# Optimization experiments

Measured on AMD Instinct MI355X. Metric: run time of the kernel, lower is better.

Reference implementation:

```python
import jax, jax.numpy as jnp
import numpy as np

B, S, D = 4, 2048, 1024


def setup_inputs() -> dict:
    key = jax.random.key(0)
    ks = jax.random.split(key, 7)
    s = 1.0 / np.sqrt(D)
    return {
        "x": jax.random.normal(ks[0], (B, S, D), dtype=jnp.float32),
        "Wq": jax.random.normal(ks[1], (D, D), dtype=jnp.float32) * s,
        "bq": jnp.zeros((D,), dtype=jnp.float32),
        "Wk": jax.random.normal(ks[2], (D, D), dtype=jnp.float32) * s,
        "bk": jnp.zeros((D,), dtype=jnp.float32),
        "Wv": jax.random.normal(ks[3], (D, D), dtype=jnp.float32) * s,
        "bv": jnp.zeros((D,), dtype=jnp.float32),
    }


def reference(x, Wq, bq, Wk, bk, Wv, bv):
    # Linear layers: x @ W^T + b (torch nn.Linear convention)
    Q = jnp.einsum("bsd,ed->bse", x, Wq) + bq
    K = jnp.einsum("bsd,ed->bse", x, Wk) + bk
    V = jnp.einsum("bsd,ed->bse", x, Wv) + bv
    scale = 1.0 / (x.shape[-1] ** 0.5)
    scores = jnp.einsum("bse,bte->bst", Q, K) * scale  # [B, S, S]
    attn = jax.nn.softmax(scores, axis=-1)
    out = jnp.einsum("bst,bte->bse", attn, V)
    return out
```

## Files before the change

kernel.cpp:

```cpp
#include <hip/hip_runtime.h>
#include <math.h>


typedef _Float16 f16;
typedef _Float16 f16x8 __attribute__((ext_vector_type(8)));
typedef _Float16 f16x4 __attribute__((ext_vector_type(4)));
typedef float f32x4 __attribute__((ext_vector_type(4)));

__device__ __forceinline__ void glds16(const void* g, const void* l) {
    __builtin_amdgcn_global_load_lds(
        (const __attribute__((address_space(1))) void*)g,
        (__attribute__((address_space(3))) void*)l, 16, 0, 0);
}

__global__ __launch_bounds__(256) void cvt16_kernel(
    const float* __restrict__ in, f16* __restrict__ o, int n4)
{
    int i = blockIdx.x * 256 + threadIdx.x;
    if (i >= n4) return;
    float4 v = ((const float4*)in)[i];
    f16x4 h = { (f16)v.x, (f16)v.y, (f16)v.z, (f16)v.w };
    ((f16x4*)o)[i] = h;
}

__global__ __launch_bounds__(256) void cvtw_kernel(
    const float* __restrict__ Wq, const float* __restrict__ Wk,
    const float* __restrict__ Wv, f16* __restrict__ o, int n4)
{
    int i = blockIdx.x * 256 + threadIdx.x;
    if (i >= n4) return;
    const float* src = (blockIdx.y == 0) ? Wq : (blockIdx.y == 1) ? Wk : Wv;
    float4 v = ((const float4*)src)[i];
    f16x4 h = { (f16)v.x, (f16)v.y, (f16)v.z, (f16)v.w };
    ((f16x4*)(o + (size_t)blockIdx.y * 1024 * 1024))[i] = h;
}

__global__ __launch_bounds__(256) void zero_kernel(float* __restrict__ p, int n)
{
    int i = blockIdx.x * 256 + threadIdx.x;
    if (i < n) p[i] = 0.0f;
}

#define ABUF 16384
#define BBUF 8192
#define BOFF 49152

__device__ __forceinline__ void mfma_core3(
    const f16* __restrict__ A, int lda,
    const f16* __restrict__ B, int ldb,
    int K, int m0, int n0, f16* sm, f32x4 acc[4][4])
{
    const int tid  = threadIdx.x;
    const int lane = tid & 63;
    const int w    = tid >> 6;
    const int wr   = w >> 1;
    const int wc   = w & 1;
    const int lr   = lane & 15;
    const int kq   = lane >> 4;

    const int rl = lane >> 3;
    const int ch = (lane & 7) ^ rl;

    const f16* gA[4];
    #pragma unroll
    for (int p = 0; p < 4; ++p)
        gA[p] = A + (size_t)(m0 + p * 64 + w * 8 + rl) * lda + ch * 8;
    const f16* gB[2];
    #pragma unroll
    for (int p = 0; p < 2; ++p)
        gB[p] = B + (size_t)(n0 + p * 64 + w * 8 + rl) * ldb + ch * 8;

    const int NT = K >> 6;

    #pragma unroll
    for (int s = 0; s < 2; ++s) {
        f16* lA = sm + s * ABUF + w * 8 * 64;
        f16* lB = sm + BOFF + s * BBUF + w * 8 * 64;
        #pragma unroll
        for (int p = 0; p < 4; ++p) glds16(gA[p] + s * 64, lA + p * 4096);
        #pragma unroll
        for (int p = 0; p < 2; ++p) glds16(gB[p] + s * 64, lB + p * 4096);
    }

    int kst = 128, sb = 2, cur = 0;
    for (int t = 0; t < NT; ++t) {
        if (t + 2 < NT) {
            f16* lA = sm + sb * ABUF + w * 8 * 64;
            f16* lB = sm + BOFF + sb * BBUF + w * 8 * 64;
            #pragma unroll
            for (int p = 0; p < 4; ++p) glds16(gA[p] + kst, lA + p * 4096);
            #pragma unroll
            for (int p = 0; p < 2; ++p) glds16(gB[p] + kst, lB + p * 4096);
            kst += 64;
            sb = (sb == 2) ? 0 : sb + 1;
        }
        if (t + 2 < NT)      asm volatile("s_waitcnt vmcnt(12)" ::: "memory");
        else if (t + 1 < NT) asm volatile("s_waitcnt vmcnt(6)"  ::: "memory");
        else                 asm volatile("s_waitcnt vmcnt(0)"  ::: "memory");
        asm volatile("s_barrier" ::: "memory");

        const f16* sA = sm + cur * ABUF;
        const f16* sB = sm + BOFF + cur * BBUF;
        #pragma unroll
        for (int kk = 0; kk < 2; ++kk) {
            f16x8 a[4], b[4];
            const int c = kk * 4 + kq;
            #pragma unroll
            for (int i = 0; i < 4; ++i) {
                const int ar = wr * 64 + i * 16 + lr;
                a[i] = *(const f16x8*)&sA[ar * 64 + ((c ^ (ar & 7)) * 8)];
            }
            #pragma unroll
            for (int j = 0; j < 4; ++j) {
                const int br = wc * 64 + j * 16 + lr;
                b[j] = *(const f16x8*)&sB[br * 64 + ((c ^ (br & 7)) * 8)];
            }
            asm volatile("s_waitcnt lgkmcnt(0)" ::: "memory");
            __builtin_amdgcn_sched_barrier(0);
            __builtin_amdgcn_s_setprio(1);
            #pragma unroll
            for (int i = 0; i < 4; ++i)
                #pragma unroll
                for (int j = 0; j < 4; ++j)
                    acc[i][j] = __builtin_amdgcn_mfma_f32_16x16x32_f16(a[i], b[j], acc[i][j], 0, 0, 0);
            __builtin_amdgcn_s_setprio(0);
            asm volatile("s_barrier" ::: "memory");
        }
        cur = (cur == 2) ? 0 : cur + 1;
    }
}

__global__ __launch_bounds__(512) void qkv_mfma_kernel(
    const f16* __restrict__ xh, const f16* __restrict__ Wh,
    const float* __restrict__ bq, const float* __restrict__ bk,
    const float* __restrict__ bv,
    f16* __restrict__ Qh, f16* __restrict__ Kh, f16* __restrict__ Vh)
{
    extern __shared__ __align__(16) f16 smem[];
    int flat = blockIdx.x + 8 * (blockIdx.y + 32 * blockIdx.z);
    flat = (flat & 7) * 96 + (flat >> 3);
    const int bx = flat & 7;
    const int by = (flat >> 3) & 31;
    const int bz = flat >> 8;

    const int m0 = by * 256;
    const int n0 = bx * 128;

    f32x4 acc[4][4];
    #pragma unroll
    for (int i = 0; i < 4; ++i)
        #pragma unroll
        for (int j = 0; j < 4; ++j) acc[i][j] = (f32x4){0.f, 0.f, 0.f, 0.f};

    mfma_core3(xh, 1024, Wh + (size_t)bz * 1024 * 1024, 1024, 1024, m0, n0, smem, acc);

    const float* bias = (bz == 0) ? bq : (bz == 1) ? bk : bv;
    const float  sc   = (bz == 0) ? 0.03125f : 1.0f;
    f16* C = (bz == 0) ? Qh : (bz == 1) ? Kh : Vh;
    const int lane = threadIdx.x & 63;
    const int w    = threadIdx.x >> 6;
    const int wr = w >> 1, wc = w & 1;
    const int col  = lane & 15;
    const int quad = lane >> 4;

    #pragma unroll
    for (int j = 0; j < 4; ++j) {
        const int gn = n0 + wc * 64 + j * 16 + col;
        const float bb = bias[gn];
        #pragma unroll
        for (int i = 0; i < 4; ++i)
            #pragma unroll
            for (int r = 0; r < 4; ++r) {
                const int gm = m0 + wr * 64 + i * 16 + quad * 4 + r;
                C[(size_t)gm * 1024 + gn] = (f16)((acc[i][j][r] + bb) * sc);
            }
    }
}

__global__ __launch_bounds__(256) void vtrans_kernel(
    const f16* __restrict__ V, f16* __restrict__ Vt)
{
    __shared__ f16 t[64][72];
    const int b  = blockIdx.z;
    const int s0 = blockIdx.x * 64;
    const int d0 = blockIdx.y * 64;
    const int tid = threadIdx.x;

    const int r  = tid >> 3;
    const int c8 = (tid & 7) * 8;
    const f16* src = V + ((size_t)b * 2048 + s0) * 1024 + d0;
    *(f16x8*)&t[r][c8]      = *(const f16x8*)(src + (size_t)r * 1024 + c8);
    *(f16x8*)&t[r + 32][c8] = *(const f16x8*)(src + (size_t)(r + 32) * 1024 + c8);
    __syncthreads();

    const int dl  = tid >> 2;
    const int sl0 = (tid & 3) * 16;
    f16* dst = Vt + ((size_t)b * 1024 + d0 + dl) * 2048 + s0 + sl0;
    f16 buf[16];
    #pragma unroll
    for (int u = 0; u < 16; ++u) buf[u] = t[sl0 + u][dl];
    *(f16x8*)dst       = *(f16x8*)&buf[0];
    *(f16x8*)(dst + 8) = *(f16x8*)&buf[8];
}

__global__ __launch_bounds__(512) void scores_exp_kernel(
    const f16* __restrict__ Qh, const f16* __restrict__ Kh,
    f16* __restrict__ P, float* __restrict__ sums)
{
    extern __shared__ __align__(16) f16 smem[];
    const int b  = blockIdx.z;
    const int m0 = blockIdx.y * 256;
    const int n0 = blockIdx.x * 128;

    f32x4 acc[4][4];
    #pragma unroll
    for (int i = 0; i < 4; ++i)
        #pragma unroll
        for (int j = 0; j < 4; ++j) acc[i][j] = (f32x4){0.f, 0.f, 0.f, 0.f};

    const size_t ao = (size_t)b * 2048 * 1024;
    mfma_core3(Qh + ao, 1024, Kh + ao, 1024, 1024, m0, n0, smem, acc);

    const int lane = threadIdx.x & 63;
    const int w    = threadIdx.x >> 6;
    const int wr = w >> 1, wc = w & 1;
    const int col  = lane & 15;
    const int quad = lane >> 4;
    f16* C = P + (size_t)b * 2048 * 2048;

    float rp[4][4];
    #pragma unroll
    for (int i = 0; i < 4; ++i)
        #pragma unroll
        for (int r = 0; r < 4; ++r) rp[i][r] = 0.0f;

    #pragma unroll
    for (int i = 0; i < 4; ++i)
        #pragma unroll
        for (int r = 0; r < 4; ++r) {
            const int gm = m0 + wr * 64 + i * 16 + quad * 4 + r;
            #pragma unroll
            for (int j = 0; j < 4; ++j) {
                const int gn = n0 + wc * 64 + j * 16 + col;
                const f16 p = (f16)__expf(acc[i][j][r]);
                C[(size_t)gm * 2048 + gn] = p;
                rp[i][r] += (float)p;
            }
        }

    #pragma unroll
    for (int i = 0; i < 4; ++i)
        #pragma unroll
        for (int r = 0; r < 4; ++r) {
            float v = rp[i][r];
            v += __shfl_xor(v, 1);
            v += __shfl_xor(v, 2);
            v += __shfl_xor(v, 4);
            v += __shfl_xor(v, 8);
            rp[i][r] = v;
        }
    if (col == 0) {
        #pragma unroll
        for (int i = 0; i < 4; ++i)
            #pragma unroll
            for (int r = 0; r < 4; ++r) {
                const int row = m0 + wr * 64 + i * 16 + quad * 4 + r;
                atomicAdd(&sums[b * 2048 + row], rp[i][r]);
            }
    }
}

__global__ __launch_bounds__(512) void pv_mfma_kernel(
    const f16* __restrict__ P, const f16* __restrict__ Vt,
    const float* __restrict__ sums, float* __restrict__ out)
{
    extern __shared__ __align__(16) f16 smem[];
    const int b  = blockIdx.z;
    const int m0 = blockIdx.y * 256;
    const int n0 = blockIdx.x * 128;

    f32x4 acc[4][4];
    #pragma unroll
    for (int i = 0; i < 4; ++i)
        #pragma unroll
        for (int j = 0; j < 4; ++j) acc[i][j] = (f32x4){0.f, 0.f, 0.f, 0.f};

    const size_t ao = (size_t)b * 2048 * 2048;
    const size_t bo = (size_t)b * 1024 * 2048;
    mfma_core3(P + ao, 2048, Vt + bo, 2048, 2048, m0, n0, smem, acc);

    const int lane = threadIdx.x & 63;
    const int w    = threadIdx.x >> 6;
    const int wr = w >> 1, wc = w & 1;
    const int col  = lane & 15;
    const int quad = lane >> 4;
    float* C = out + (size_t)b * 2048 * 1024;

    #pragma unroll
    for (int i = 0; i < 4; ++i)
        #pragma unroll
        for (int r = 0; r < 4; ++r) {
            const int rowg = m0 + wr * 64 + i * 16 + quad * 4 + r;
            const float inv = 1.0f / sums[b * 2048 + rowg];
            #pragma unroll
            for (int j = 0; j < 4; ++j) {
                const int gn = n0 + wc * 64 + j * 16 + col;
                C[(size_t)rowg * 1024 + gn] = acc[i][j][r] * inv;
            }
        }
}

extern "C" void kernel_launch(void* const* d_in, const int* in_sizes, int n_in,
                              void* d_out, int out_size, void* d_ws, size_t ws_size,
                              hipStream_t stream)
{
    (void)in_sizes; (void)n_in; (void)out_size; (void)ws_size;
    const int Bn = 4, S = 2048, D = 1024;
    const float* x  = (const float*)d_in[0];
    const float* Wq = (const float*)d_in[1];
    const float* bq = (const float*)d_in[2];
    const float* Wk = (const float*)d_in[3];
    const float* bk = (const float*)d_in[4];
    const float* Wv = (const float*)d_in[5];
    const float* bv = (const float*)d_in[6];
    float* out = (float*)d_out;

    const size_t MB = 1024 * 1024;
    char* w = (char*)d_ws;
    f16*   xh   = (f16*)(w + 0 * MB);
    f16*   Wh3  = (f16*)(w + 16 * MB);
    f16*   Vh   = (f16*)(w + 22 * MB);
    f16*   Qh   = (f16*)(w + 38 * MB);
    f16*   Kh   = (f16*)(w + 54 * MB);
    f16*   Vt   = (f16*)(w + 70 * MB);
    float* sums = (float*)(w + 86 * MB);
    f16*   P    = (f16*)(w + 0 * MB);

    static bool attr_set = false;
    if (!attr_set) {
        hipFuncSetAttribute(reinterpret_cast<const void*>(qkv_mfma_kernel),
                            hipFuncAttributeMaxDynamicSharedMemorySize, 147456);
        hipFuncSetAttribute(reinterpret_cast<const void*>(scores_exp_kernel),
                            hipFuncAttributeMaxDynamicSharedMemorySize, 147456);
        hipFuncSetAttribute(reinterpret_cast<const void*>(pv_mfma_kernel),
                            hipFuncAttributeMaxDynamicSharedMemorySize, 147456);
        attr_set = true;
    }

    cvt16_kernel<<<dim3(Bn * S * D / 4 / 256), 256, 0, stream>>>(x, xh, Bn * S * D / 4);
    cvtw_kernel<<<dim3(D * D / 4 / 256, 3), 256, 0, stream>>>(Wq, Wk, Wv, Wh3, D * D / 4);
    zero_kernel<<<dim3((Bn * S + 255) / 256), 256, 0, stream>>>(sums, Bn * S);

    qkv_mfma_kernel<<<dim3(D / 128, (Bn * S) / 256, 3), 512, 147456, stream>>>(
        xh, Wh3, bq, bk, bv, Qh, Kh, Vh);
    vtrans_kernel<<<dim3(S / 64, D / 64, Bn), 256, 0, stream>>>(Vh, Vt);

    scores_exp_kernel<<<dim3(S / 128, S / 256, Bn), 512, 147456, stream>>>(
        Qh, Kh, P, sums);
    pv_mfma_kernel<<<dim3(D / 128, S / 256, Bn), 512, 147456, stream>>>(
        P, Vt, sums, out);
}
```

Measured before the change: 267.1 us.

## Software-pipeline LDS fragment reads with MFMA and swizzle block order for L2 locality

Restructures the shared GEMM mainloop so the next tile's LDS fragments are read into registers while MFMAs run on the current tile, using double register buffers and a two-step unrolled loop with rotating LDS stage pointers. It also remaps block indices in the scores and PV kernels into an XCD-aware interleaved order, and adds a min-waves-per-EU hint of 2 to launch bounds. The aim is to hide LDS latency and raise cache locality, at the cost of more registers, which could conflict with the occupancy hint and cause spills. Shared memory of 144 KB per block may already limit residency to one block per CU.

```diff
diff --git a/kernel.cpp b/kernel.cpp
--- a/kernel.cpp
+++ b/kernel.cpp
@@ -12,6 +12,11 @@
         (const __attribute__((address_space(1))) void*)g,
         (__attribute__((address_space(3))) void*)l, 16, 0, 0);
 }
+
+#define VMCNT(n)  asm volatile("s_waitcnt vmcnt(" #n ")" ::: "memory")
+#define LGKM(n)   asm volatile("s_waitcnt lgkmcnt(" #n ")" ::: "memory")
+#define BARRIER() asm volatile("s_barrier" ::: "memory")
+#define SCHEDB()  __builtin_amdgcn_sched_barrier(0)
 
 __global__ __launch_bounds__(256) void cvt16_kernel(
     const float* __restrict__ in, f16* __restrict__ o, int n4)
@@ -44,6 +49,38 @@
 #define ABUF 16384
 #define BBUF 8192
 #define BOFF 49152
+
+__device__ __forceinline__ void frag_read16(
+    const f16* __restrict__ sA, const f16* __restrict__ sB,
+    int wr, int wc, int lr, int kq, f16x8 a[2][4], f16x8 b[2][4])
+{
+    #pragma unroll
+    for (int kk = 0; kk < 2; ++kk) {
+        const int c = kk * 4 + kq;
+        #pragma unroll
+        for (int i = 0; i < 4; ++i) {
+            const int ar = wr * 64 + i * 16 + lr;
+            a[kk][i] = *(const f16x8*)&sA[ar * 64 + ((c ^ (ar & 7)) * 8)];
+        }
+        #pragma unroll
+        for (int j = 0; j < 4; ++j) {
+            const int br = wc * 64 + j * 16 + lr;
+            b[kk][j] = *(const f16x8*)&sB[br * 64 + ((c ^ (br & 7)) * 8)];
+        }
+    }
+}
+
+__device__ __forceinline__ void mfma32(
+    const f16x8 a[2][4], const f16x8 b[2][4], f32x4 acc[4][4])
+{
+    #pragma unroll
+    for (int kk = 0; kk < 2; ++kk)
+        #pragma unroll
+        for (int i = 0; i < 4; ++i)
+            #pragma unroll
+            for (int j = 0; j < 4; ++j)
+                acc[i][j] = __builtin_amdgcn_mfma_f32_16x16x32_f16(a[kk][i], b[kk][j], acc[i][j], 0, 0, 0);
+}
 
 __device__ __forceinline__ void mfma_core3(
     const f16* __restrict__ A, int lda,
@@ -72,65 +109,62 @@
 
     const int NT = K >> 6;
 
-    #pragma unroll
-    for (int s = 0; s < 2; ++s) {
-        f16* lA = sm + s * ABUF + w * 8 * 64;
-        f16* lB = sm + BOFF + s * BBUF + w * 8 * 64;
-        #pragma unroll
-        for (int p = 0; p < 4; ++p) glds16(gA[p] + s * 64, lA + p * 4096);
-        #pragma unroll
-        for (int p = 0; p < 2; ++p) glds16(gB[p] + s * 64, lB + p * 4096);
+    f16* sA0 = sm;             f16* sB0 = sm + BOFF;
+    f16* sA1 = sm + ABUF;      f16* sB1 = sm + BOFF + BBUF;
+    f16* sA2 = sm + 2 * ABUF;  f16* sB2 = sm + BOFF + 2 * BBUF;
+
+    #define STAGE(kofs, dA, dB) do {                                          \
+        _Pragma("unroll")                                                     \
+        for (int p = 0; p < 4; ++p)                                           \
+            glds16(gA[p] + (kofs), (dA) + w * 512 + p * 4096);                \
+        _Pragma("unroll")                                                     \
+        for (int p = 0; p < 2; ++p)                                           \
+            glds16(gB[p] + (kofs), (dB) + w * 512 + p * 4096);                \
+    } while (0)
+
+    STAGE(0,  sA0, sB0);
+    STAGE(64, sA1, sB1);
+    VMCNT(6);
+    BARRIER();
+    f16x8 a0[2][4], b0[2][4], a1[2][4], b1[2][4];
+    frag_read16(sA0, sB0, wr, wc, lr, kq, a0, b0);
+
+    for (int t = 0; t < NT; t += 2) {
+        if (t + 2 < NT) { STAGE((t + 2) * 64, sA2, sB2); VMCNT(6); }
+        else            { VMCNT(0); }
+        BARRIER();
+        frag_read16(sA1, sB1, wr, wc, lr, kq, a1, b1);
+        LGKM(15);
+        SCHEDB();
+        __builtin_amdgcn_s_setprio(1);
+        mfma32(a0, b0, acc);
+        __builtin_amdgcn_s_setprio(0);
+        BARRIER();
+
+        if (t + 3 < NT) { STAGE((t + 3) * 64, sA0, sB0); }
+        if (t + 2 < NT) {
+            if (t + 3 < NT) { VMCNT(6); } else { VMCNT(0); }
+        }
+        BARRIER();
+        if (t + 2 < NT) {
+            frag_read16(sA2, sB2, wr, wc, lr, kq, a0, b0);
+            LGKM(15);
+        } else {
+            LGKM(0);
+        }
+        SCHEDB();
+        __builtin_amdgcn_s_setprio(1);
+        mfma32(a1, b1, acc);
+        __builtin_amdgcn_s_setprio(0);
+        BARRIER();
+
+        f16* tA = sA2; sA2 = sA1; sA1 = sA0; sA0 = tA;
+        f16* tB = sB2; sB2 = sB1; sB1 = sB0; sB0 = tB;
     }
-
-    int kst = 128, sb = 2, cur = 0;
-    for (int t = 0; t < NT; ++t) {
-        if (t + 2 < NT) {
-            f16* lA = sm + sb * ABUF + w * 8 * 64;
-            f16* lB = sm + BOFF + sb * BBUF + w * 8 * 64;
-            #pragma unroll
-            for (int p = 0; p < 4; ++p) glds16(gA[p] + kst, lA + p * 4096);
-            #pragma unroll
-            for (int p = 0; p < 2; ++p) glds16(gB[p] + kst, lB + p * 4096);
-            kst += 64;
-            sb = (sb == 2) ? 0 : sb + 1;
-        }
-        if (t + 2 < NT)      asm volatile("s_waitcnt vmcnt(12)" ::: "memory");
-        else if (t + 1 < NT) asm volatile("s_waitcnt vmcnt(6)"  ::: "memory");
-        else                 asm volatile("s_waitcnt vmcnt(0)"  ::: "memory");
-        asm volatile("s_barrier" ::: "memory");
-
-        const f16* sA = sm + cur * ABUF;
-        const f16* sB = sm + BOFF + cur * BBUF;
-        #pragma unroll
-        for (int kk = 0; kk < 2; ++kk) {
-            f16x8 a[4], b[4];
-            const int c = kk * 4 + kq;
-            #pragma unroll
-            for (int i = 0; i < 4; ++i) {
-                const int ar = wr * 64 + i * 16 + lr;
-                a[i] = *(const f16x8*)&sA[ar * 64 + ((c ^ (ar & 7)) * 8)];
-            }
-            #pragma unroll
-            for (int j = 0; j < 4; ++j) {
-                const int br = wc * 64 + j * 16 + lr;
-                b[j] = *(const f16x8*)&sB[br * 64 + ((c ^ (br & 7)) * 8)];
-            }
-            asm volatile("s_waitcnt lgkmcnt(0)" ::: "memory");
-            __builtin_amdgcn_sched_barrier(0);
-            __builtin_amdgcn_s_setprio(1);
-            #pragma unroll
-            for (int i = 0; i < 4; ++i)
-                #pragma unroll
-                for (int j = 0; j < 4; ++j)
-                    acc[i][j] = __builtin_amdgcn_mfma_f32_16x16x32_f16(a[i], b[j], acc[i][j], 0, 0, 0);
-            __builtin_amdgcn_s_setprio(0);
-            asm volatile("s_barrier" ::: "memory");
-        }
-        cur = (cur == 2) ? 0 : cur + 1;
-    }
-}
-
-__global__ __launch_bounds__(512) void qkv_mfma_kernel(
+    #undef STAGE
+}
+
+__global__ __launch_bounds__(512, 2) void qkv_mfma_kernel(
     const f16* __restrict__ xh, const f16* __restrict__ Wh,
     const float* __restrict__ bq, const float* __restrict__ bk,
     const float* __restrict__ bv,
@@ -203,14 +237,19 @@
     *(f16x8*)(dst + 8) = *(f16x8*)&buf[8];
 }
 
-__global__ __launch_bounds__(512) void scores_exp_kernel(
+__global__ __launch_bounds__(512, 2) void scores_exp_kernel(
     const f16* __restrict__ Qh, const f16* __restrict__ Kh,
     f16* __restrict__ P, float* __restrict__ sums)
 {
     extern __shared__ __align__(16) f16 smem[];
-    const int b  = blockIdx.z;
-    const int m0 = blockIdx.y * 256;
-    const int n0 = blockIdx.x * 128;
+    int flat = blockIdx.x + 16 * (blockIdx.y + 8 * blockIdx.z);
+    flat = (flat & 7) * 64 + (flat >> 3);
+    const int bx = flat & 15;
+    const int by = (flat >> 4) & 7;
+    const int b  = flat >> 7;
+
+    const int m0 = by * 256;
+    const int n0 = bx * 128;
 
     f32x4 acc[4][4];
     #pragma unroll
@@ -270,14 +309,19 @@
     }
 }
 
-__global__ __launch_bounds__(512) void pv_mfma_kernel(
+__global__ __launch_bounds__(512, 2) void pv_mfma_kernel(
     const f16* __restrict__ P, const f16* __restrict__ Vt,
     const float* __restrict__ sums, float* __restrict__ out)
 {
     extern __shared__ __align__(16) f16 smem[];
-    const int b  = blockIdx.z;
-    const int m0 = blockIdx.y * 256;
-    const int n0 = blockIdx.x * 128;
+    int flat = blockIdx.x + 8 * (blockIdx.y + 8 * blockIdx.z);
+    flat = (flat & 7) * 32 + (flat >> 3);
+    const int bx = flat & 7;
+    const int by = (flat >> 3) & 7;
+    const int b  = flat >> 6;
+
+    const int m0 = by * 256;
+    const int n0 = bx * 128;
 
     f32x4 acc[4][4];
     #pragma unroll
@@ -338,11 +382,11 @@
 
     static bool attr_set = false;
     if (!attr_set) {
-        hipFuncSetAttribute(reinterpret_cast<const void*>(qkv_mfma_kernel),
+        (void)hipFuncSetAttribute(reinterpret_cast<const void*>(qkv_mfma_kernel),
                             hipFuncAttributeMaxDynamicSharedMemorySize, 147456);
-        hipFuncSetAttribute(reinterpret_cast<const void*>(scores_exp_kernel),
+        (void)hipFuncSetAttribute(reinterpret_cast<const void*>(scores_exp_kernel),
                             hipFuncAttributeMaxDynamicSharedMemorySize, 147456);
-        hipFuncSetAttribute(reinterpret_cast<const void*>(pv_mfma_kernel),
+        (void)hipFuncSetAttribute(reinterpret_cast<const void*>(pv_mfma_kernel),
                             hipFuncAttributeMaxDynamicSharedMemorySize, 147456);
         attr_set = true;
     }
```

New measurement: 267.9 us. About the same (+0.3%).

## Fuse prep kernels and write V transposed directly from QKV epilogue

Applied to the files above, without the earlier changes.

Merges the x/W fp16 conversion and the sums zeroing into one prep kernel, cutting two launches. The QKV GEMM epilogue for the V plane now writes V transposed (f16x4 along sequence) straight into Vt, removing the separate transpose kernel and the round trip of V through memory. The mfma pipeline swaps buffer-index arithmetic for rotating pointers. The transposed stores are strided by 2048 elements per column, which may coalesce worse than the old row-major writes.

```diff
diff --git a/kernel.cpp b/kernel.cpp
--- a/kernel.cpp
+++ b/kernel.cpp
@@ -13,32 +13,36 @@
         (__attribute__((address_space(3))) void*)l, 16, 0, 0);
 }
 
-__global__ __launch_bounds__(256) void cvt16_kernel(
-    const float* __restrict__ in, f16* __restrict__ o, int n4)
-{
-    int i = blockIdx.x * 256 + threadIdx.x;
-    if (i >= n4) return;
-    float4 v = ((const float4*)in)[i];
-    f16x4 h = { (f16)v.x, (f16)v.y, (f16)v.z, (f16)v.w };
-    ((f16x4*)o)[i] = h;
-}
-
-__global__ __launch_bounds__(256) void cvtw_kernel(
+#define VMCNT(n)  asm volatile("s_waitcnt vmcnt(" #n ")" ::: "memory")
+#define LGKM(n)   asm volatile("s_waitcnt lgkmcnt(" #n ")" ::: "memory")
+#define BARRIER() asm volatile("s_barrier" ::: "memory")
+#define SCHEDB()  __builtin_amdgcn_sched_barrier(0)
+
+__global__ __launch_bounds__(256) void prep_kernel(
+    const float* __restrict__ x,
     const float* __restrict__ Wq, const float* __restrict__ Wk,
-    const float* __restrict__ Wv, f16* __restrict__ o, int n4)
-{
-    int i = blockIdx.x * 256 + threadIdx.x;
-    if (i >= n4) return;
-    const float* src = (blockIdx.y == 0) ? Wq : (blockIdx.y == 1) ? Wk : Wv;
-    float4 v = ((const float4*)src)[i];
-    f16x4 h = { (f16)v.x, (f16)v.y, (f16)v.z, (f16)v.w };
-    ((f16x4*)(o + (size_t)blockIdx.y * 1024 * 1024))[i] = h;
-}
-
-__global__ __launch_bounds__(256) void zero_kernel(float* __restrict__ p, int n)
-{
-    int i = blockIdx.x * 256 + threadIdx.x;
-    if (i < n) p[i] = 0.0f;
+    const float* __restrict__ Wv,
+    f16* __restrict__ xh, f16* __restrict__ Wh3, float* __restrict__ sums)
+{
+    const int bid = blockIdx.x, tid = threadIdx.x;
+    if (bid < 8) {
+        float4 z = {0.f, 0.f, 0.f, 0.f};
+        ((float4*)sums)[bid * 256 + tid] = z;
+    }
+    if (bid < 8192) {
+        const int i = bid * 256 + tid;
+        float4 v = ((const float4*)x)[i];
+        f16x4 h = { (f16)v.x, (f16)v.y, (f16)v.z, (f16)v.w };
+        ((f16x4*)xh)[i] = h;
+    } else {
+        const int wid   = bid - 8192;
+        const int plane = wid >> 10;
+        const int i     = (wid & 1023) * 256 + tid;
+        const float* src = (plane == 0) ? Wq : (plane == 1) ? Wk : Wv;
+        float4 v = ((const float4*)src)[i];
+        f16x4 h = { (f16)v.x, (f16)v.y, (f16)v.z, (f16)v.w };
+        ((f16x4*)(Wh3 + (size_t)plane * 1024 * 1024))[i] = h;
+    }
 }
 
 #define ABUF 16384
@@ -72,51 +76,55 @@
 
     const int NT = K >> 6;
 
-    #pragma unroll
-    for (int s = 0; s < 2; ++s) {
-        f16* lA = sm + s * ABUF + w * 8 * 64;
-        f16* lB = sm + BOFF + s * BBUF + w * 8 * 64;
-        #pragma unroll
-        for (int p = 0; p < 4; ++p) glds16(gA[p] + s * 64, lA + p * 4096);
-        #pragma unroll
-        for (int p = 0; p < 2; ++p) glds16(gB[p] + s * 64, lB + p * 4096);
-    }
-
-    int kst = 128, sb = 2, cur = 0;
+    f16* sA0 = sm;             f16* sB0 = sm + BOFF;
+    f16* sA1 = sm + ABUF;      f16* sB1 = sm + BOFF + BBUF;
+    f16* sA2 = sm + 2 * ABUF;  f16* sB2 = sm + BOFF + 2 * BBUF;
+
+    #define STAGE(kofs, dA, dB) do {                                          \
+        _Pragma("unroll")                                                     \
+        for (int p = 0; p < 4; ++p)                                           \
+            glds16(gA[p] + (kofs), (dA) + w * 512 + p * 4096);                \
+        _Pragma("unroll")                                                     \
+        for (int p = 0; p < 2; ++p)                                           \
+            glds16(gB[p] + (kofs), (dB) + w * 512 + p * 4096);                \
+    } while (0)
+
+    STAGE(0,  sA0, sB0);
+    STAGE(64, sA1, sB1);
+
+    int kst = 128;
+    f16* curA = sA0; f16* curB = sB0;
+    f16* nxtA = sA1; f16* nxtB = sB1;
+    f16* farA = sA2; f16* farB = sB2;
+
     for (int t = 0; t < NT; ++t) {
         if (t + 2 < NT) {
-            f16* lA = sm + sb * ABUF + w * 8 * 64;
-            f16* lB = sm + BOFF + sb * BBUF + w * 8 * 64;
-            #pragma unroll
-            for (int p = 0; p < 4; ++p) glds16(gA[p] + kst, lA + p * 4096);
-            #pragma unroll
-            for (int p = 0; p < 2; ++p) glds16(gB[p] + kst, lB + p * 4096);
+            STAGE(kst, farA, farB);
             kst += 64;
-            sb = (sb == 2) ? 0 : sb + 1;
-        }
-        if (t + 2 < NT)      asm volatile("s_waitcnt vmcnt(12)" ::: "memory");
-        else if (t + 1 < NT) asm volatile("s_waitcnt vmcnt(6)"  ::: "memory");
-        else                 asm volatile("s_waitcnt vmcnt(0)"  ::: "memory");
-        asm volatile("s_barrier" ::: "memory");
-
-        const f16* sA = sm + cur * ABUF;
-        const f16* sB = sm + BOFF + cur * BBUF;
+            VMCNT(12);
+        } else if (t + 1 < NT) {
+            VMCNT(6);
+        } else {
+            VMCNT(0);
+        }
+        BARRIER();
+
         #pragma unroll
         for (int kk = 0; kk < 2; ++kk) {
             f16x8 a[4], b[4];
             const int c = kk * 4 + kq;
             #pragma unroll
             for (int i = 0; i < 4; ++i) {
-                const int ar = wr * 64 + i * 16 + lr;
-                a[i] = *(const f16x8*)&sA[ar * 64 + ((c ^ (ar & 7)) * 8)];
+                const int ra = wr * 64 + i * 16 + lr;
+                a[i] = *(const f16x8*)&curA[ra * 64 + ((c ^ (ra & 7)) * 8)];
             }
             #pragma unroll
             for (int j = 0; j < 4; ++j) {
-                const int br = wc * 64 + j * 16 + lr;
-                b[j] = *(const f16x8*)&sB[br * 64 + ((c ^ (br & 7)) * 8)];
-            }
-            asm volatile("s_waitcnt lgkmcnt(0)" ::: "memory");
-            __builtin_amdgcn_sched_barrier(0);
+                const int rb = wc * 64 + j * 16 + lr;
+                b[j] = *(const f16x8*)&curB[rb * 64 + ((c ^ (rb & 7)) * 8)];
+            }
+            LGKM(0);
+            SCHEDB();
             __builtin_amdgcn_s_setprio(1);
             #pragma unroll
             for (int i = 0; i < 4; ++i)
@@ -124,17 +132,22 @@
                 for (int j = 0; j < 4; ++j)
                     acc[i][j] = __builtin_amdgcn_mfma_f32_16x16x32_f16(a[i], b[j], acc[i][j], 0, 0, 0);
             __builtin_amdgcn_s_setprio(0);
-            asm volatile("s_barrier" ::: "memory");
-        }
-        cur = (cur == 2) ? 0 : cur + 1;
-    }
+            BARRIER();
+        }
+
+        f16* tA = curA; f16* tB = curB;
+        curA = nxtA; curB = nxtB;
+        nxtA = farA; nxtB = farB;
+        farA = tA;   farB = tB;
+    }
+    #undef STAGE
 }
 
 __global__ __launch_bounds__(512) void qkv_mfma_kernel(
     const f16* __restrict__ xh, const f16* __restrict__ Wh,
     const float* __restrict__ bq, const float* __restrict__ bk,
     const float* __restrict__ bv,
-    f16* __restrict__ Qh, f16* __restrict__ Kh, f16* __restrict__ Vh)
+    f16* __restrict__ Qh, f16* __restrict__ Kh, f16* __restrict__ Vt)
 {
     extern __shared__ __align__(16) f16 smem[];
     int flat = blockIdx.x + 8 * (blockIdx.y + 32 * blockIdx.z);
@@ -154,53 +167,46 @@
 
     mfma_core3(xh, 1024, Wh + (size_t)bz * 1024 * 1024, 1024, 1024, m0, n0, smem, acc);
 
-    const float* bias = (bz == 0) ? bq : (bz == 1) ? bk : bv;
-    const float  sc   = (bz == 0) ? 0.03125f : 1.0f;
-    f16* C = (bz == 0) ? Qh : (bz == 1) ? Kh : Vh;
     const int lane = threadIdx.x & 63;
     const int w    = threadIdx.x >> 6;
-    const int wr = w >> 1, wc = w & 1;
+    const int wm = (w >> 1) * 64;
+    const int wn = (w & 1) * 64;
     const int col  = lane & 15;
     const int quad = lane >> 4;
 
-    #pragma unroll
-    for (int j = 0; j < 4; ++j) {
-        const int gn = n0 + wc * 64 + j * 16 + col;
-        const float bb = bias[gn];
-        #pragma unroll
-        for (int i = 0; i < 4; ++i)
-            #pragma unroll
-            for (int r = 0; r < 4; ++r) {
-                const int gm = m0 + wr * 64 + i * 16 + quad * 4 + r;
-                C[(size_t)gm * 1024 + gn] = (f16)((acc[i][j][r] + bb) * sc);
-            }
-    }
-}
-
-__global__ __launch_bounds__(256) void vtrans_kernel(
-    const f16* __restrict__ V, f16* __restrict__ Vt)
-{
-    __shared__ f16 t[64][72];
-    const int b  = blockIdx.z;
-    const int s0 = blockIdx.x * 64;
-    const int d0 = blockIdx.y * 64;
-    const int tid = threadIdx.x;
-
-    const int r  = tid >> 3;
-    const int c8 = (tid & 7) * 8;
-    const f16* src = V + ((size_t)b * 2048 + s0) * 1024 + d0;
-    *(f16x8*)&t[r][c8]      = *(const f16x8*)(src + (size_t)r * 1024 + c8);
-    *(f16x8*)&t[r + 32][c8] = *(const f16x8*)(src + (size_t)(r + 32) * 1024 + c8);
-    __syncthreads();
-
-    const int dl  = tid >> 2;
-    const int sl0 = (tid & 3) * 16;
-    f16* dst = Vt + ((size_t)b * 1024 + d0 + dl) * 2048 + s0 + sl0;
-    f16 buf[16];
-    #pragma unroll
-    for (int u = 0; u < 16; ++u) buf[u] = t[sl0 + u][dl];
-    *(f16x8*)dst       = *(f16x8*)&buf[0];
-    *(f16x8*)(dst + 8) = *(f16x8*)&buf[8];
+    if (bz == 2) {
+        #pragma unroll
+        for (int i = 0; i < 4; ++i) {
+            const int gmb = m0 + wm + i * 16 + quad * 4;
+            const int bb_ = gmb >> 11;
+            const int s   = gmb & 2047;
+            f16* vtb = Vt + (size_t)bb_ * 1024 * 2048;
+            #pragma unroll
+            for (int j = 0; j < 4; ++j) {
+                const int gn = n0 + wn + j * 16 + col;
+                const float bbv = bv[gn];
+                f16x4 v = { (f16)(acc[i][j][0] + bbv), (f16)(acc[i][j][1] + bbv),
+                            (f16)(acc[i][j][2] + bbv), (f16)(acc[i][j][3] + bbv) };
+                *(f16x4*)&vtb[(size_t)gn * 2048 + s] = v;
+            }
+        }
+    } else {
+        const float* bias = (bz == 0) ? bq : bk;
+        const float  sc   = (bz == 0) ? 0.03125f : 1.0f;
+        f16* C = (bz == 0) ? Qh : Kh;
+        #pragma unroll
+        for (int j = 0; j < 4; ++j) {
+            const int gn = n0 + wn + j * 16 + col;
+            const float bb = bias[gn];
+            #pragma unroll
+            for (int i = 0; i < 4; ++i)
+                #pragma unroll
+                for (int r = 0; r < 4; ++r) {
+                    const int gm = m0 + wm + i * 16 + quad * 4 + r;
+                    C[(size_t)gm * 1024 + gn] = (f16)((acc[i][j][r] + bb) * sc);
+                }
+        }
+    }
 }
 
 __global__ __launch_bounds__(512) void scores_exp_kernel(
@@ -223,7 +229,8 @@
 
     const int lane = threadIdx.x & 63;
     const int w    = threadIdx.x >> 6;
-    const int wr = w >> 1, wc = w & 1;
+    const int wm = (w >> 1) * 64;
+    const int wn = (w & 1) * 64;
     const int col  = lane & 15;
     const int quad = lane >> 4;
     f16* C = P + (size_t)b * 2048 * 2048;
@@ -238,10 +245,10 @@
     for (int i = 0; i < 4; ++i)
         #pragma unroll
         for (int r = 0; r < 4; ++r) {
-            const int gm = m0 + wr * 64 + i * 16 + quad * 4 + r;
+            const int gm = m0 + wm + i * 16 + quad * 4 + r;
             #pragma unroll
             for (int j = 0; j < 4; ++j) {
-                const int gn = n0 + wc * 64 + j * 16 + col;
+                const int gn = n0 + wn + j * 16 + col;
                 const f16 p = (f16)__expf(acc[i][j][r]);
                 C[(size_t)gm * 2048 + gn] = p;
                 rp[i][r] += (float)p;
@@ -264,7 +271,7 @@
         for (int i = 0; i < 4; ++i)
             #pragma unroll
             for (int r = 0; r < 4; ++r) {
-                const int row = m0 + wr * 64 + i * 16 + quad * 4 + r;
+                const int row = m0 + wm + i * 16 + quad * 4 + r;
                 atomicAdd(&sums[b * 2048 + row], rp[i][r]);
             }
     }
@@ -291,7 +298,8 @@
 
     const int lane = threadIdx.x & 63;
     const int w    = threadIdx.x >> 6;
-    const int wr = w >> 1, wc = w & 1;
+    const int wm = (w >> 1) * 64;
+    const int wn = (w & 1) * 64;
     const int col  = lane & 15;
     const int quad = lane >> 4;
     float* C = out + (size_t)b * 2048 * 1024;
@@ -300,12 +308,12 @@
     for (int i = 0; i < 4; ++i)
         #pragma unroll
         for (int r = 0; r < 4; ++r) {
-            const int rowg = m0 + wr * 64 + i * 16 + quad * 4 + r;
-            const float inv = 1.0f / sums[b * 2048 + rowg];
+            const int rl = m0 + wm + i * 16 + quad * 4 + r;
+            const float inv = 1.0f / sums[b * 2048 + rl];
             #pragma unroll
             for (int j = 0; j < 4; ++j) {
-                const int gn = n0 + wc * 64 + j * 16 + col;
-                C[(size_t)rowg * 1024 + gn] = acc[i][j][r] * inv;
+                const int gn = n0 + wn + j * 16 + col;
+                C[(size_t)rl * 1024 + gn] = acc[i][j][r] * inv;
             }
         }
 }
@@ -329,7 +337,6 @@
     char* w = (char*)d_ws;
     f16*   xh   = (f16*)(w + 0 * MB);
     f16*   Wh3  = (f16*)(w + 16 * MB);
-    f16*   Vh   = (f16*)(w + 22 * MB);
     f16*   Qh   = (f16*)(w + 38 * MB);
     f16*   Kh   = (f16*)(w + 54 * MB);
     f16*   Vt   = (f16*)(w + 70 * MB);
@@ -338,22 +345,19 @@
 
     static bool attr_set = false;
     if (!attr_set) {
-        hipFuncSetAttribute(reinterpret_cast<const void*>(qkv_mfma_kernel),
+        (void)hipFuncSetAttribute(reinterpret_cast<const void*>(qkv_mfma_kernel),
                             hipFuncAttributeMaxDynamicSharedMemorySize, 147456);
-        hipFuncSetAttribute(reinterpret_cast<const void*>(scores_exp_kernel),
+        (void)hipFuncSetAttribute(reinterpret_cast<const void*>(scores_exp_kernel),
                             hipFuncAttributeMaxDynamicSharedMemorySize, 147456);
-        hipFuncSetAttribute(reinterpret_cast<const void*>(pv_mfma_kernel),
+        (void)hipFuncSetAttribute(reinterpret_cast<const void*>(pv_mfma_kernel),
                             hipFuncAttributeMaxDynamicSharedMemorySize, 147456);
         attr_set = true;
     }
 
-    cvt16_kernel<<<dim3(Bn * S * D / 4 / 256), 256, 0, stream>>>(x, xh, Bn * S * D / 4);
-    cvtw_kernel<<<dim3(D * D / 4 / 256, 3), 256, 0, stream>>>(Wq, Wk, Wv, Wh3, D * D / 4);
-    zero_kernel<<<dim3((Bn * S + 255) / 256), 256, 0, stream>>>(sums, Bn * S);
+    prep_kernel<<<dim3(11264), 256, 0, stream>>>(x, Wq, Wk, Wv, xh, Wh3, sums);
 
     qkv_mfma_kernel<<<dim3(D / 128, (Bn * S) / 256, 3), 512, 147456, stream>>>(
-        xh, Wh3, bq, bk, bv, Qh, Kh, Vh);
-    vtrans_kernel<<<dim3(S / 64, D / 64, Bn), 256, 0, stream>>>(Vh, Vt);
+        xh, Wh3, bq, bk, bv, Qh, Kh, Vt);
 
     scores_exp_kernel<<<dim3(S / 128, S / 256, Bn), 512, 147456, stream>>>(
         Qh, Kh, P, sums);
```

Measured after the change: 260.8 us. 2.4% less time.
